# Kernel tuning notes

Hardware: AMD Instinct MI355X
Metric: run time of the kernel (lower is better)

## Reference

```python
import jax, jax.numpy as jnp
import numpy as np

E, H, O = 300, 256, 2            # embedding_size, hidden_size, output_size
N_SENT, SENT_LEN, CLAIM_LEN = 2048, 64, 64


def setup_inputs() -> dict:
    key = jax.random.key(0)
    ks = jax.random.split(key, 24)
    rn = lambda k, shape, s=0.05: (jax.random.normal(k, shape, jnp.float32) * s)
    return {
        "claim": jax.random.normal(ks[0], (CLAIM_LEN, E), jnp.float32),
        "sentences": jax.random.normal(ks[1], (N_SENT, SENT_LEN, E), jnp.float32),
        # claim GRU (PyTorch layout: W_ih (3H,E), W_hh (3H,H), gates ordered r,z,n)
        "Wih_c": rn(ks[2], (3 * H, E)), "Whh_c": rn(ks[3], (3 * H, H)),
        "bih_c": rn(ks[4], (3 * H,)), "bhh_c": rn(ks[5], (3 * H,)),
        # sentence GRU
        "Wih_s": rn(ks[6], (3 * H, E)), "Whh_s": rn(ks[7], (3 * H, H)),
        "bih_s": rn(ks[8], (3 * H,)), "bhh_s": rn(ks[9], (3 * H,)),
        # gates (no bias)
        "Wg_s": rn(ks[10], (1, H)), "Wg_c": rn(ks[11], (1, H)),
        # coherence attention
        "Wac": rn(ks[12], (H, H)), "bac": rn(ks[13], (H,)),
        "Was": rn(ks[14], (1, H)), "bas": rn(ks[15], (1,)),
        # extension linear (H, 2H)
        "Wext": rn(ks[16], (H, 2 * H)), "bext": rn(ks[17], (H,)),
        # joint linear (H, 4H), no bias
        "Wj": rn(ks[18], (H, 4 * H)),
        # entailment attention
        "Wae": rn(ks[19], (1, H)), "bae": rn(ks[20], (1,)),
        # final classifier
        "Wf": rn(ks[21], (O, H)), "bf": rn(ks[22], (O,)),
    }


def _gru_last(x, Wih, Whh, bih, bhh):
    """x: (T, B, E) -> final hidden state (B, H). PyTorch GRU math, zero init."""
    B = x.shape[1]
    Hd = Whh.shape[1]
    gi = jnp.einsum('tbe,ge->tbg', x, Wih) + bih  # (T, B, 3H), input projections

    def step(h, gi_t):
        gh = h @ Whh.T + bhh
        ir, iz, inn = jnp.split(gi_t, 3, axis=-1)
        hr, hz, hn = jnp.split(gh, 3, axis=-1)
        r = jax.nn.sigmoid(ir + hr)
        z = jax.nn.sigmoid(iz + hz)
        n = jnp.tanh(inn + r * hn)
        return (1.0 - z) * n + z * h, None

    h0 = jnp.zeros((B, Hd), x.dtype)
    hT, _ = jax.lax.scan(step, h0, gi)
    return hT


def reference(claim, sentences, Wih_c, Whh_c, bih_c, bhh_c,
              Wih_s, Whh_s, bih_s, bhh_s, Wg_s, Wg_c,
              Wac, bac, Was, bas, Wext, bext, Wj, Wae, bae, Wf, bf):
    # claim encoder: (T,1,E) -> hc (1,H)
    hc = _gru_last(claim[:, None, :], Wih_c, Whh_c, bih_c, bhh_c)
    # batched sentence encoder (replaces the per-sentence Python loop)
    HS = _gru_last(jnp.transpose(sentences, (1, 0, 2)), Wih_s, Whh_s, bih_s, bhh_s)  # (N,H)
    # gated fusion of sentence reps with claim rep
    g = jax.nn.sigmoid(HS @ Wg_s.T + hc @ Wg_c.T)          # (N,1)
    HSg = g * HS + (1.0 - g) * hc                           # (N,H)
    # coherence attention over sentences (row-wise softmax)
    scores = (HSg @ Wac.T + bac) @ HSg.T + (HSg @ Was.T + bas)  # (N,N)
    coh = jax.nn.softmax(scores, axis=1)
    H_apo = coh @ HSg                                       # (N,H)
    H_tilde = jnp.tanh(jnp.concatenate([HS, H_apo], axis=1) @ Wext.T + bext)  # (N,H)
    # joint claim-sentence entailment features (replaces per-row loop)
    hc_b = jnp.broadcast_to(hc, H_tilde.shape)
    joint_in = jnp.concatenate(
        [hc_b, H_tilde, hc * H_tilde, jnp.abs(hc - H_tilde)], axis=1)  # (N,4H)
    H_c_s = jnp.tanh(joint_in @ Wj.T)                       # (N,H)
    # entailment attention (softmax over sentence axis)
    ae = jnp.tanh(H_c_s @ Wae.T + bae)                      # (N,1)
    w = jax.nn.softmax(ae, axis=0)                          # (N,1)
    h_c_S = w.T @ H_c_s                                     # (1,H)
    return jax.nn.sigmoid(h_c_S @ Wf.T + bf)                # (1,O)
```

## Files before the change

kernel.cpp:

```cpp
#include <hip/hip_runtime.h>

typedef unsigned short u16;
typedef unsigned int u32;
typedef short bf16x8 __attribute__((ext_vector_type(8)));
typedef float f32x4 __attribute__((ext_vector_type(4)));
typedef u16 u16x4v __attribute__((ext_vector_type(4)));

__device__ __forceinline__ float b2f(u16 h){ return __uint_as_float(((unsigned)h)<<16); }
__device__ __forceinline__ u16 f2b(float f){
  unsigned u = __float_as_uint(f);
  u += 0x7fffu + ((u>>16)&1u);
  return (u16)(u>>16);
}
__device__ __forceinline__ float sigm(float x){ return 1.f/(1.f+__expf(-x)); }
__device__ __forceinline__ float tanh_(float x){
  float ax=fabsf(x), e=__expf(-2.f*ax), t=(1.f-e)/(1.f+e);
  return x<0.f? -t : t;
}
__device__ __forceinline__ bf16x8 ld8a(const u16* p){
  union{ u16x4v h[2]; bf16x8 v; } u;
  u.h[0]=*(const u16x4v*)p; u.h[1]=*(const u16x4v*)(p+4); return u.v;
}
__device__ __forceinline__ f32x4 mfma16(bf16x8 a, bf16x8 b, f32x4 c){
  return __builtin_amdgcn_mfma_f32_16x16x32_bf16(a,b,c,0,0,0);
}

#define VMW(N)  do{ asm volatile("s_waitcnt vmcnt(" #N ")" ::: "memory"); \
                    __builtin_amdgcn_sched_barrier(0); }while(0)
#define LGK0    do{ asm volatile("s_waitcnt lgkmcnt(0)" ::: "memory"); \
                    __builtin_amdgcn_sched_barrier(0); }while(0)
#define BAR()   do{ asm volatile("" ::: "memory"); __builtin_amdgcn_s_barrier(); \
                    asm volatile("" ::: "memory"); __builtin_amdgcn_sched_barrier(0); }while(0)

__device__ __forceinline__ void gl_lds16(const void* g, void* s){
  __builtin_amdgcn_global_load_lds(
      (const __attribute__((address_space(1))) void*)g,
      (__attribute__((address_space(3))) void*)s, 16, 0, 0);
}
__device__ __forceinline__ void stage_rows(const u16* base, int ld, int kc,
                                           u16* buf, int w, int l){
  #pragma unroll
  for (int ii=0; ii<6; ii++){
    const int i   = w + ii*8;
    const int row = i*16 + (l>>2);
    const int c8  = (l&3) ^ ((row>>2)&3);
    gl_lds16(base + (long)row*ld + kc*32 + c8*8, buf + i*512);
  }
}
__device__ __forceinline__ bf16x8 ldB(const u16* buf, int row, int l){
  const int slot = (l>>4) ^ ((row>>2)&3);
  return *(const bf16x8*)((const char*)buf + row*64 + slot*16);
}

__global__ __launch_bounds__(256) void cvt_kernel(
    const float* __restrict__ WihS, const float* __restrict__ WhhS,
    const float* __restrict__ WihC, const float* __restrict__ WhhC,
    const float* __restrict__ Wac,  const float* __restrict__ Wext,
    const float* __restrict__ Wj,
    const float* __restrict__ bihS, const float* __restrict__ bhhS,
    const float* __restrict__ bihC, const float* __restrict__ bhhC,
    u16* __restrict__ WihP, u16* __restrict__ WhhSb,
    u16* __restrict__ WihCP, u16* __restrict__ WhhCb,
    u16* __restrict__ WacB, u16* __restrict__ WextB, u16* __restrict__ WjB,
    float* __restrict__ biasGI, float* __restrict__ biasGIC)
{
  const int seg = blockIdx.y;
  int n;
  switch(seg){
    case 0: n = 768*320; break;  case 1: n = 196608; break;
    case 2: n = 768*320; break;  case 3: n = 196608; break;
    case 4: n = 65536; break;    case 5: n = 131072; break;
    case 6: n = 262144; break;   default: n = 1536; break;
  }
  for (int i = blockIdx.x*256 + threadIdx.x; i < n; i += gridDim.x*256){
    switch(seg){
      case 0: { int r=i/320, c=i-r*320; WihP[i]  = (c<300)? f2b(WihS[r*300+c]) : (u16)0; } break;
      case 1: WhhSb[i] = f2b(WhhS[i]); break;
      case 2: { int r=i/320, c=i-r*320; WihCP[i] = (c<300)? f2b(WihC[r*300+c]) : (u16)0; } break;
      case 3: WhhCb[i] = f2b(WhhC[i]); break;
      case 4: WacB[i]  = f2b(Wac[i]);  break;
      case 5: WextB[i] = f2b(Wext[i]); break;
      case 6: WjB[i]   = f2b(Wj[i]);   break;
      default:
        if (i < 768) biasGI[i] = bihS[i] + (i < 512 ? bhhS[i] : 0.f);
        else { int j = i - 768; biasGIC[j] = bihC[j] + (j < 512 ? bhhC[j] : 0.f); }
        break;
    }
  }
}

__global__ __launch_bounds__(512) void gi_kernel(
    const int pass,
    const float* __restrict__ sents, const float* __restrict__ claim,
    const u16* __restrict__ WihP, const float* __restrict__ biasGI,
    const u16* __restrict__ WihCP, const float* __restrict__ biasGIC,
    u16* __restrict__ gi_b, float* __restrict__ giC)
{
  __shared__ __align__(16) u16 SA[64*320];
  __shared__ __align__(16) u16 BB[2][768*32];
  const int tid=threadIdx.x, w=tid>>6, l=tid&63, ar=l&15, kg8=(l>>4)*8;
  const f32x4 z4 = {0.f,0.f,0.f,0.f};
  const bool isClaim = (blockIdx.x == 1024);
  const int b = blockIdx.x;

  for (int i=tid; i<64*80; i+=512){
    int r = i/80, q = i - r*80;
    u16x4v o;
    if (q < 75){
      float4 v;
      if (!isClaim) v = ((const float4*)sents)[(long)(2*b + (r>>5))*4800 + (pass*32 + (r&31))*75 + q];
      else          v = ((const float4*)claim)[r*75 + q];
      o[0]=f2b(v.x); o[1]=f2b(v.y); o[2]=f2b(v.z); o[3]=f2b(v.w);
    } else { o[0]=0; o[1]=0; o[2]=0; o[3]=0; }
    int byte = r*640 + q*8; byte ^= (r&7)<<4;
    *(u16x4v*)((char*)SA + byte) = o;
  }
  const u16* Bw = isClaim ? WihCP : WihP;
  stage_rows(Bw, 320, 0, BB[0], w, l);
  stage_rows(Bw, 320, 1, BB[1], w, l);
  LGK0;
  BAR();

  f32x4 acc[24];
  #pragma unroll
  for (int q=0;q<24;q++) acc[q]=z4;

  #pragma unroll
  for (int kc=0;kc<10;kc++){
    if (kc==9) VMW(0); else VMW(6);
    BAR();
    bf16x8 bq[6];
    #pragma unroll
    for (int q=0;q<6;q++) bq[q] = ldB(BB[kc&1], w*96 + q*16 + ar, l);
    #pragma unroll
    for (int m=0;m<4;m++){
      const int abyte = ((m*16+ar)*640 + (kc*32+kg8)*2) ^ ((ar&7)<<4);
      const bf16x8 a = *(const bf16x8*)((const char*)SA + abyte);
      #pragma unroll
      for (int q=0;q<6;q++) acc[m*6+q] = mfma16(a, bq[q], acc[m*6+q]);
    }
    BAR();
    if (kc<8) stage_rows(Bw, 320, kc+2, BB[kc&1], w, l);
  }
  VMW(0);
  const int rb = (l>>4)*4;
  if (!isClaim){
    #pragma unroll
    for (int q=0;q<6;q++){
      const int c = w*96 + q*16 + ar;
      const float bs = biasGI[c];
      #pragma unroll
      for (int m=0;m<4;m++)
        #pragma unroll
        for (int p=0;p<4;p++)
          gi_b[(long)(b*64 + m*16 + rb + p)*768 + c] = f2b(acc[m*6+q][p] + bs);
    }
  } else {
    #pragma unroll
    for (int q=0;q<6;q++){
      const int c = w*96 + q*16 + ar;
      const float bs = biasGIC[c];
      #pragma unroll
      for (int m=0;m<4;m++)
        #pragma unroll
        for (int p=0;p<4;p++)
          giC[(m*16 + rb + p)*768 + c] = acc[m*6+q][p] + bs;
    }
  }
}

__global__ __launch_bounds__(512) void rec_kernel(
    const int pass,
    const u16* __restrict__ gi_b, const u16* __restrict__ WhhSb,
    const float* __restrict__ bhhS,
    float* __restrict__ Hmid, u16* __restrict__ HSout,
    const float* __restrict__ giC, const u16* __restrict__ WhhCb,
    const float* __restrict__ bhhC, const float* __restrict__ Wj,
    const float* __restrict__ WgC,
    float* __restrict__ hcMid, float* __restrict__ hcf,
    float* __restrict__ cvec, float* __restrict__ c0p)
{
  __shared__ __align__(16) u16 Hb[2][16][256];
  __shared__ __align__(16) u16 giL[2][8][776];
  __shared__ float ghL[768];
  __shared__ float hfL[256];
  __shared__ __align__(16) u16 hbL[256];
  const int tid=threadIdx.x, w=tid>>6, l=tid&63, ar=l&15, kg8=(l>>4)*8;
  const f32x4 z4 = {0.f,0.f,0.f,0.f};

  asm volatile("" ::: "v250");

  if (blockIdx.x != 0){
    const long i0 = (long)(blockIdx.x - 1)*8;
    const int rb = (l>>4)*4;
    bf16x8 wf[6][8];
    #pragma unroll
    for (int s=0;s<3;s++)
      #pragma unroll
      for (int ti=0;ti<2;ti++)
        #pragma unroll
        for (int kc=0;kc<8;kc++)
          wf[s*2+ti][kc] = ld8a(WhhSb + (s*256 + w*32 + ti*16 + ar)*256 + kc*32 + kg8);
    const float bhn0 = bhhS[512 + w*32 +  0 + ar];
    const float bhn1 = bhhS[512 + w*32 + 16 + ar];

    for (int i=tid; i<2*16*256; i+=512) ((u16*)Hb)[i] = 0;
    __syncthreads();
    float hold[2][4];
    #pragma unroll
    for (int ti=0;ti<2;ti++)
      #pragma unroll
      for (int p=0;p<4;p++) hold[ti][p] = 0.f;
    if (pass==1 && l<32){
      #pragma unroll
      for (int ti=0;ti<2;ti++){
        #pragma unroll
        for (int p=0;p<4;p++){
          const int c = w*32 + ti*16 + ar, rr = rb + p;
          const float h = Hmid[(i0+rr)*256 + c];
          hold[ti][p] = h;
          const int byte = (rr*512 + c*2) ^ ((rr&7)<<4);
          *(u16*)((char*)&Hb[0][0][0] + byte) = f2b(h);
        }
      }
    }
    const u32* g32 = (const u32*)gi_b;
    u32 pf[6];
    #pragma unroll
    for (int rep=0;rep<6;rep++){
      const int i = rep*512 + tid, j = i/384, cu = i - j*384;
      pf[rep] = g32[((i0+j)*32 + 0)*384 + cu];
    }
    #pragma unroll
    for (int rep=0;rep<6;rep++){
      const int i = rep*512 + tid, j = i/384, cu = i - j*384;
      *(u32*)((char*)&giL[0][0][0] + j*1552 + cu*4) = pf[rep];
    }
    __syncthreads();

    int cur = 0;
    for (int tl=0; tl<32; tl++){
      const int tn = (tl<31) ? tl+1 : 31;
      #pragma unroll
      for (int rep=0;rep<6;rep++){
        const int i = rep*512 + tid, j = i/384, cu = i - j*384;
        pf[rep] = g32[((i0+j)*32 + tn)*384 + cu];
      }
      f32x4 acc[6];
      #pragma unroll
      for (int q=0;q<6;q++) acc[q]=z4;
      if (l < 32){
        #pragma unroll
        for (int s=0;s<2;s++)
          #pragma unroll
          for (int ti=0;ti<2;ti++)
            #pragma unroll
            for (int p=0;p<4;p++){
              const int c = w*32 + ti*16 + ar;
              const u16 v = *(const u16*)((const char*)&giL[cur][0][0] + (rb+p)*1552 + (s*256+c)*2);
              acc[s*2+ti][p] = b2f(v);
            }
      }
      #pragma unroll
      for (int kc=0;kc<8;kc++){
        const int abyte = (ar*512 + (kc*32+kg8)*2) ^ ((ar&7)<<4);
        const bf16x8 a = *(const bf16x8*)((const char*)&Hb[cur][0][0] + abyte);
        #pragma unroll
        for (int q=0;q<6;q++) acc[q] = mfma16(a, wf[q][kc], acc[q]);
      }
      #pragma unroll
      for (int rep=0;rep<6;rep++){
        const int i = rep*512 + tid, j = i/384, cu = i - j*384;
        *(u32*)((char*)&giL[cur^1][0][0] + j*1552 + cu*4) = pf[rep];
      }
      if (l < 32){
        #pragma unroll
        for (int ti=0;ti<2;ti++){
          const int c = w*32 + ti*16 + ar;
          const float bhn = ti ? bhn1 : bhn0;
          #pragma unroll
          for (int p=0;p<4;p++){
            const int rr = rb + p;
            const u16 gv = *(const u16*)((const char*)&giL[cur][0][0] + rr*1552 + (512+c)*2);
            const float r_ = sigm(acc[0+ti][p]);
            const float z_ = sigm(acc[2+ti][p]);
            const float n_ = tanh_(b2f(gv) + r_*(acc[4+ti][p] + bhn));
            const float h = (1.f - z_)*n_ + z_*hold[ti][p];
            hold[ti][p] = h;
            const int byte = (rr*512 + c*2) ^ ((rr&7)<<4);
            *(u16*)((char*)&Hb[cur^1][0][0] + byte) = f2b(h);
          }
        }
      }
      __syncthreads();
      cur ^= 1;
    }
    if (l < 32){
      #pragma unroll
      for (int ti=0;ti<2;ti++){
        #pragma unroll
        for (int p=0;p<4;p++){
          const int c = w*32 + ti*16 + ar, rr = rb + p;
          if (pass==0) Hmid[(i0+rr)*256 + c] = hold[ti][p];
          else         HSout[(i0+rr)*512 + c] = f2b(hold[ti][p]);
        }
      }
    }
  } else {
    const u16* wrow[6];
    #pragma unroll
    for (int q=0;q<6;q++) wrow[q] = WhhCb + (w*96 + q*16 + ar)*256 + kg8;
    if (tid < 256){
      const float h0 = (pass==0) ? 0.f : hcMid[tid];
      hfL[tid] = h0; hbL[tid] = f2b(h0);
    }
    __syncthreads();
    for (int tl=0; tl<32; tl++){
      const int t = pass*32 + tl;
      f32x4 a6[6];
      #pragma unroll
      for (int q=0;q<6;q++) a6[q]=z4;
      #pragma unroll
      for (int kc=0;kc<8;kc++){
        bf16x8 wq[6];
        #pragma unroll
        for (int q=0;q<6;q++) wq[q] = ld8a(wrow[q] + kc*32);
        const bf16x8 a = ld8a((const u16*)hbL + kc*32 + kg8);
        #pragma unroll
        for (int q=0;q<6;q++) a6[q] = mfma16(a, wq[q], a6[q]);
      }
      if (l < 16){
        #pragma unroll
        for (int q=0;q<6;q++) ghL[w*96 + q*16 + l] = a6[q][0];
      }
      __syncthreads();
      if (tid < 256){
        const int c = tid;
        const float r_ = sigm(giC[t*768 +       c] + ghL[c]);
        const float z_ = sigm(giC[t*768 + 256 + c] + ghL[256 + c]);
        const float n_ = tanh_(giC[t*768 + 512 + c] + r_*(ghL[512 + c] + bhhC[512 + c]));
        const float h = (1.f - z_)*n_ + z_*hfL[c];
        hfL[c] = h; hbL[c] = f2b(h);
      }
      __syncthreads();
    }
    if (tid < 256){
      const int c = tid;
      const float hv = hfL[c];
      if (pass == 0) hcMid[c] = hv;
      else {
        hcf[c] = hv;
        float acc2 = 0.f;
        for (int k=0;k<256;k++) acc2 += hfL[k]*Wj[(long)c*1024 + k];
        cvec[c] = acc2;
        if (c==0){ float s=0.f; for (int k=0;k<256;k++) s += hfL[k]*WgC[k]; *c0p = s; }
      }
    }
  }
}

__global__ __launch_bounds__(256) void fusion_kernel(
    const u16* __restrict__ HSH, const float* __restrict__ Wgs,
    const float* __restrict__ hcf, const float* __restrict__ c0p,
    u16* __restrict__ HSg, u16* __restrict__ HSgT)
{
  __shared__ float gbuf[64];
  __shared__ __align__(16) u16 tile[64][258];
  const int tid=threadIdx.x, w=tid>>6, l=tid&63;
  const long i0 = (long)blockIdx.x * 64;
  const float c0 = *c0p;
  for (int rr=0; rr<16; rr++){
    long i = i0 + w*16 + rr;
    float p = 0.f;
    for (int c=l; c<256; c+=64) p += b2f(HSH[i*512+c]) * Wgs[c];
    for (int o=32;o;o>>=1) p += __shfl_down(p,o,64);
    if (l==0) gbuf[w*16+rr] = sigm(p + c0);
  }
  __syncthreads();
  for (int idx=tid; idx<64*256; idx+=256){
    int r = idx>>8, c = idx&255;
    float g = gbuf[r];
    float hs = b2f(HSH[(i0+r)*512 + c]);
    u16 bv = f2b(g*hs + (1.f-g)*hcf[c]);
    HSg[(i0+r)*256 + c] = bv;
    tile[r][c] = bv;
  }
  __syncthreads();
  const int ioff = tid&63, cg = tid>>6;
  for (int cc=cg; cc<256; cc+=4)
    HSgT[(long)cc*2048 + i0 + ioff] = tile[ioff][cc];
}

template<int MODE>
__global__ __launch_bounds__(256) void gemmk(
    const u16* __restrict__ A, long lda,
    const u16* __restrict__ Bw, long ldb,
    void* __restrict__ Cp, long ldc, int K,
    const float* __restrict__ biasf,
    const float* __restrict__ hc)
{
  const int tid=threadIdx.x, w=tid>>6, l=tid&63, ar=l&15, kg8=(l>>4)*8;
  const long row0 = (long)blockIdx.x*64 + w*16;
  const long col0 = (long)blockIdx.y*64;
  const f32x4 z4 = {0.f,0.f,0.f,0.f};
  f32x4 acc[4] = {z4,z4,z4,z4};
  const u16* ap = A + (row0+ar)*lda + kg8;
  const u16* bp0 = Bw + (col0+ 0+ar)*ldb + kg8;
  const u16* bp1 = Bw + (col0+16+ar)*ldb + kg8;
  const u16* bp2 = Bw + (col0+32+ar)*ldb + kg8;
  const u16* bp3 = Bw + (col0+48+ar)*ldb + kg8;
  for (int k0=0; k0<K; k0+=32){
    bf16x8 a = ld8a(ap + k0);
    acc[0] = mfma16(a, ld8a(bp0+k0), acc[0]);
    acc[1] = mfma16(a, ld8a(bp1+k0), acc[1]);
    acc[2] = mfma16(a, ld8a(bp2+k0), acc[2]);
    acc[3] = mfma16(a, ld8a(bp3+k0), acc[3]);
  }
  const int rbase = (l>>4)*4;
  #pragma unroll
  for (int t=0;t<4;t++){
    long c = col0 + t*16 + ar;
    #pragma unroll
    for (int p=0;p<4;p++){
      long r = row0 + rbase + p;
      float v = acc[t][p];
      if constexpr (MODE==0){
        if (biasf) v += biasf[c];
        ((u16*)Cp)[r*ldc + c] = f2b(v);
      } else if constexpr (MODE==1){
        ((float*)Cp)[r*ldc + c] = v;
      } else if constexpr (MODE==2){
        float tv = tanh_(v + biasf[c]);
        u16* Uo = (u16*)Cp;
        float hv = hc[c];
        Uo[r*768 + c]       = f2b(tv);
        Uo[r*768 + 256 + c] = f2b(hv*tv);
        Uo[r*768 + 512 + c] = f2b(fabsf(hv - tv));
      } else {
        float tv = tanh_(v + biasf[c]);
        ((u16*)Cp)[r*ldc + c] = f2b(tv);
      }
    }
  }
}

__global__ __launch_bounds__(256) void softmax_rows(float* __restrict__ S)
{
  __shared__ float buf[2048];
  __shared__ float red[4];
  const long i = blockIdx.x;
  float* row = S + i*2048;
  const int tid = threadIdx.x;
  float m = -1e30f;
  for (int c=tid; c<2048; c+=256){ float v=row[c]; buf[c]=v; m=fmaxf(m,v); }
  for (int o=32;o;o>>=1) m = fmaxf(m, __shfl_down(m,o,64));
  if ((tid&63)==0) red[tid>>6] = m;
  __syncthreads();
  m = fmaxf(fmaxf(red[0],red[1]), fmaxf(red[2],red[3]));
  __syncthreads();
  float s = 0.f;
  for (int c=tid; c<2048; c+=256){ float e=__expf(buf[c]-m); buf[c]=e; s+=e; }
  for (int o=32;o;o>>=1) s += __shfl_down(s,o,64);
  if ((tid&63)==0) red[tid>>6] = s;
  __syncthreads();
  s = red[0]+red[1]+red[2]+red[3];
  const float rinv = 1.f/s;
  u16* P = (u16*)S + i*4096;
  for (int c=tid; c<2048; c+=256) P[c] = f2b(buf[c]*rinv);
}

__global__ __launch_bounds__(256) void ae_kernel(
    const u16* __restrict__ Hcs, const float* __restrict__ Wae, const float* __restrict__ bae,
    float* __restrict__ part, float* __restrict__ psum)
{
  __shared__ float aebuf[64];
  const int b=blockIdx.x, tid=threadIdx.x, w=tid>>6, l=tid&63;
  const long i0 = (long)b*64;
  const float baev = bae[0];
  for (int rr=0; rr<16; rr++){
    long i = i0 + w*16 + rr;
    float p = 0.f;
    for (int c=l; c<256; c+=64) p += b2f(Hcs[i*256+c]) * Wae[c];
    for (int o=32;o;o>>=1) p += __shfl_down(p,o,64);
    if (l==0) aebuf[w*16+rr] = __expf(tanh_(p + baev));
  }
  __syncthreads();
  float acc = 0.f;
  const int c = tid;
  for (int r=0;r<64;r++) acc += aebuf[r] * b2f(Hcs[(i0+r)*256 + c]);
  part[b*256 + c] = acc;
  if (tid==0){ float s=0.f; for (int r=0;r<64;r++) s+=aebuf[r]; psum[b]=s; }
}

__global__ __launch_bounds__(256) void final_kernel(
    const float* __restrict__ part, const float* __restrict__ psum,
    const float* __restrict__ Wf, const float* __restrict__ bf_, float* __restrict__ out)
{
  __shared__ float hbuf[256];
  __shared__ float ssum;
  const int tid = threadIdx.x;
  float v = 0.f;
  for (int b=0;b<32;b++) v += part[b*256 + tid];
  hbuf[tid] = v;
  if (tid==0){ float s=0.f; for (int b=0;b<32;b++) s+=psum[b]; ssum=s; }
  __syncthreads();
  const int w = tid>>6, l = tid&63;
  if (w < 2){
    float rinv = 1.f/ssum;
    float p = 0.f;
    for (int c=l; c<256; c+=64) p += hbuf[c]*rinv*Wf[w*256 + c];
    for (int o=32;o;o>>=1) p += __shfl_down(p,o,64);
    if (l==0) out[w] = sigm(p + bf_[w]);
  }
}

extern "C" void kernel_launch(void* const* d_in, const int* in_sizes, int n_in,
                              void* d_out, int out_size, void* d_ws, size_t ws_size,
                              hipStream_t stream)
{
  const float* claim=(const float*)d_in[0];
  const float* sents=(const float*)d_in[1];
  const float* WihC =(const float*)d_in[2];
  const float* WhhC =(const float*)d_in[3];
  const float* bihC =(const float*)d_in[4];
  const float* bhhC =(const float*)d_in[5];
  const float* WihS =(const float*)d_in[6];
  const float* WhhS =(const float*)d_in[7];
  const float* bihS =(const float*)d_in[8];
  const float* bhhS =(const float*)d_in[9];
  const float* WgS  =(const float*)d_in[10];
  const float* WgC  =(const float*)d_in[11];
  const float* Wac  =(const float*)d_in[12];
  const float* bac  =(const float*)d_in[13];
  const float* Wext =(const float*)d_in[16];
  const float* bext =(const float*)d_in[17];
  const float* Wj   =(const float*)d_in[18];
  const float* Wae  =(const float*)d_in[19];
  const float* bae  =(const float*)d_in[20];
  const float* Wf   =(const float*)d_in[21];
  const float* bf_  =(const float*)d_in[22];

  char* ws = (char*)d_ws;
  size_t off = 0;
  auto alloc = [&](size_t b)->void*{ void* p = ws + off; off = (off + b + 255) & ~(size_t)255; return p; };
  float* hcf  = (float*)alloc(256*4);
  float* cvec = (float*)alloc(256*4);
  float* c0p  = (float*)alloc(16);
  float* hcMid= (float*)alloc(256*4);
  float* giC  = (float*)alloc((size_t)64*768*4);
  u16* WihP   = (u16*)alloc((size_t)768*320*2);
  u16* WhhSb  = (u16*)alloc((size_t)196608*2);
  u16* WihCP  = (u16*)alloc((size_t)768*320*2);
  u16* WhhCb  = (u16*)alloc((size_t)196608*2);
  u16* WacB   = (u16*)alloc((size_t)65536*2);
  u16* WextB  = (u16*)alloc((size_t)131072*2);
  u16* WjB    = (u16*)alloc((size_t)262144*2);
  float* biasGI  = (float*)alloc(768*4);
  float* biasGIC = (float*)alloc(768*4);
  u16* HSH  = (u16*)alloc((size_t)2048*512*2);
  u16* HSg  = (u16*)alloc((size_t)2048*256*2);
  u16* HSgT = (u16*)alloc((size_t)256*2048*2);
  u16* A1   = (u16*)alloc((size_t)2048*256*2);
  u16* Up   = (u16*)alloc((size_t)2048*768*2);
  u16* Hcs  = (u16*)alloc((size_t)2048*256*2);
  float* part = (float*)alloc(32*256*4);
  float* psum = (float*)alloc(32*4);
  float* Hmid = (float*)alloc((size_t)2048*256*4);
  u16* gi_b   = (u16*)alloc((size_t)65536*768*2);
  float* S    = (float*)gi_b;

  cvt_kernel<<<dim3(960,8),256,0,stream>>>(WihS,WhhS,WihC,WhhC,Wac,Wext,Wj,
                                           bihS,bhhS,bihC,bhhC,
                                           WihP,WhhSb,WihCP,WhhCb,WacB,WextB,WjB,
                                           biasGI,biasGIC);
  gi_kernel<<<1025,512,0,stream>>>(0,sents,claim,WihP,biasGI,WihCP,biasGIC,gi_b,giC);
  rec_kernel<<<257,512,0,stream>>>(0,gi_b,WhhSb,bhhS,Hmid,HSH,
                                   giC,WhhCb,bhhC,Wj,WgC,hcMid,hcf,cvec,c0p);
  gi_kernel<<<1024,512,0,stream>>>(1,sents,claim,WihP,biasGI,WihCP,biasGIC,gi_b,giC);
  rec_kernel<<<257,512,0,stream>>>(1,gi_b,WhhSb,bhhS,Hmid,HSH,
                                   giC,WhhCb,bhhC,Wj,WgC,hcMid,hcf,cvec,c0p);

  fusion_kernel<<<32,256,0,stream>>>(HSH,WgS,hcf,c0p,HSg,HSgT);
  gemmk<0><<<dim3(32,4),256,0,stream>>>(HSg,256L,WacB,256L,(void*)A1,256L,256,bac,nullptr);
  gemmk<1><<<dim3(32,32),256,0,stream>>>(A1,256L,HSg,256L,(void*)S,2048L,256,nullptr,nullptr);
  softmax_rows<<<2048,256,0,stream>>>(S);
  gemmk<0><<<dim3(32,4),256,0,stream>>>((const u16*)S,4096L,HSgT,2048L,(void*)(HSH+256),512L,2048,nullptr,nullptr);
  gemmk<2><<<dim3(32,4),256,0,stream>>>(HSH,512L,WextB,512L,(void*)Up,768L,512,bext,hcf);
  gemmk<3><<<dim3(32,4),256,0,stream>>>(Up,768L,WjB+256,1024L,(void*)Hcs,256L,768,cvec,nullptr);
  ae_kernel<<<32,256,0,stream>>>(Hcs,Wae,bae,part,psum);
  final_kernel<<<1,256,0,stream>>>(part,psum,Wf,bf_,(float*)d_out);
}
```

Before: 800.5 us.

## Overlap second-half input projection with first-half GRU recurrence in one launch

Adds a combined kernel in which blocks 1-256 run the first 32 timesteps of the sentence GRU recurrence while extra blocks (257+) compute the input-gate projections for timesteps 32-63 into a second buffer. This lets the latency-bound recurrence share the GPU with the compute-bound GEMM instead of running them back to back. It needs a second large gi buffer and falls back to the old sequence when workspace is too small. Co-scheduled projection blocks may contend for CUs and memory bandwidth with the recurrence blocks.

Result: slower. 861.0 us (+7.6%).

```diff
diff --git a/kernel.cpp b/kernel.cpp
--- a/kernel.cpp
+++ b/kernel.cpp
@@ -187,7 +187,6 @@
   __shared__ __align__(16) u16 hbL[256];
   const int tid=threadIdx.x, w=tid>>6, l=tid&63, ar=l&15, kg8=(l>>4)*8;
   const f32x4 z4 = {0.f,0.f,0.f,0.f};
-
   asm volatile("" ::: "v250");
 
   if (blockIdx.x != 0){
@@ -356,6 +355,209 @@
         if (c==0){ float s=0.f; for (int k=0;k<256;k++) s += hfL[k]*WgC[k]; *c0p = s; }
       }
     }
+  }
+}
+
+__global__ __launch_bounds__(512) void recgi_kernel(
+    const u16* __restrict__ gi_bA, const u16* __restrict__ WhhSb,
+    const float* __restrict__ bhhS, float* __restrict__ Hmid,
+    const float* __restrict__ giC, const u16* __restrict__ WhhCb,
+    const float* __restrict__ bhhC, float* __restrict__ hcMid,
+    const float* __restrict__ sents, const u16* __restrict__ WihP,
+    const float* __restrict__ biasGI, u16* __restrict__ gi_bB)
+{
+  __shared__ __align__(16) char SM[45824];
+  const int tid=threadIdx.x, w=tid>>6, l=tid&63, ar=l&15, kg8=(l>>4)*8;
+  const f32x4 z4 = {0.f,0.f,0.f,0.f};
+  asm volatile("" ::: "v250");
+
+  if (blockIdx.x >= 257){
+    u16* SA = (u16*)SM;
+    const int b = blockIdx.x - 257;
+    for (int i=tid; i<64*80; i+=512){
+      int r = i/80, q = i - r*80;
+      u16x4v o;
+      if (q < 75){
+        const float4 v = ((const float4*)sents)[(long)(2*b + (r>>5))*4800 + (32 + (r&31))*75 + q];
+        o[0]=f2b(v.x); o[1]=f2b(v.y); o[2]=f2b(v.z); o[3]=f2b(v.w);
+      } else { o[0]=0; o[1]=0; o[2]=0; o[3]=0; }
+      int byte = r*640 + q*8; byte ^= (r&7)<<4;
+      *(u16x4v*)((char*)SA + byte) = o;
+    }
+    __syncthreads();
+    const u16* brow[6];
+    #pragma unroll
+    for (int q=0;q<6;q++) brow[q] = WihP + (w*96 + q*16 + ar)*320 + kg8;
+    f32x4 acc[24];
+    #pragma unroll
+    for (int q=0;q<24;q++) acc[q]=z4;
+    #pragma unroll
+    for (int kc=0;kc<10;kc++){
+      bf16x8 bq[6];
+      #pragma unroll
+      for (int q=0;q<6;q++) bq[q] = ld8a(brow[q] + kc*32);
+      #pragma unroll
+      for (int m=0;m<4;m++){
+        const int abyte = ((m*16+ar)*640 + (kc*32+kg8)*2) ^ ((ar&7)<<4);
+        const bf16x8 a = *(const bf16x8*)((const char*)SA + abyte);
+        #pragma unroll
+        for (int q=0;q<6;q++) acc[m*6+q] = mfma16(a, bq[q], acc[m*6+q]);
+      }
+    }
+    const int rb = (l>>4)*4;
+    #pragma unroll
+    for (int q=0;q<6;q++){
+      const int c = w*96 + q*16 + ar;
+      const float bs = biasGI[c];
+      #pragma unroll
+      for (int m=0;m<4;m++)
+        #pragma unroll
+        for (int p=0;p<4;p++)
+          gi_bB[(long)(b*64 + m*16 + rb + p)*768 + c] = f2b(acc[m*6+q][p] + bs);
+    }
+  } else if (blockIdx.x != 0){
+    u16*  HbP  = (u16*)SM;
+    u16*  giLp = (u16*)(SM + 16384);
+    const long i0 = (long)(blockIdx.x - 1)*8;
+    const int rb = (l>>4)*4;
+    bf16x8 wf[6][8];
+    #pragma unroll
+    for (int s=0;s<3;s++)
+      #pragma unroll
+      for (int ti=0;ti<2;ti++)
+        #pragma unroll
+        for (int kc=0;kc<8;kc++)
+          wf[s*2+ti][kc] = ld8a(WhhSb + (s*256 + w*32 + ti*16 + ar)*256 + kc*32 + kg8);
+    const float bhn0 = bhhS[512 + w*32 +  0 + ar];
+    const float bhn1 = bhhS[512 + w*32 + 16 + ar];
+
+    for (int i=tid; i<2*16*256; i+=512) HbP[i] = 0;
+    __syncthreads();
+    float hold[2][4];
+    #pragma unroll
+    for (int ti=0;ti<2;ti++)
+      #pragma unroll
+      for (int p=0;p<4;p++) hold[ti][p] = 0.f;
+    const u32* g32 = (const u32*)gi_bA;
+    u32 pf[6];
+    #pragma unroll
+    for (int rep=0;rep<6;rep++){
+      const int i = rep*512 + tid, j = i/384, cu = i - j*384;
+      pf[rep] = g32[((i0+j)*32 + 0)*384 + cu];
+    }
+    #pragma unroll
+    for (int rep=0;rep<6;rep++){
+      const int i = rep*512 + tid, j = i/384, cu = i - j*384;
+      *(u32*)((char*)giLp + j*1552 + cu*4) = pf[rep];
+    }
+    __syncthreads();
+
+    int cur = 0;
+    for (int tl=0; tl<32; tl++){
+      const int tn = (tl<31) ? tl+1 : 31;
+      #pragma unroll
+      for (int rep=0;rep<6;rep++){
+        const int i = rep*512 + tid, j = i/384, cu = i - j*384;
+        pf[rep] = g32[((i0+j)*32 + tn)*384 + cu];
+      }
+      f32x4 acc[6];
+      #pragma unroll
+      for (int q=0;q<6;q++) acc[q]=z4;
+      if (l < 32){
+        #pragma unroll
+        for (int s=0;s<2;s++)
+          #pragma unroll
+          for (int ti=0;ti<2;ti++)
+            #pragma unroll
+            for (int p=0;p<4;p++){
+              const int c = w*32 + ti*16 + ar;
+              const u16 v = *(const u16*)((const char*)giLp + cur*12416 + (rb+p)*1552 + (s*256+c)*2);
+              acc[s*2+ti][p] = b2f(v);
+            }
+      }
+      #pragma unroll
+      for (int kc=0;kc<8;kc++){
+        const int abyte = (ar*512 + (kc*32+kg8)*2) ^ ((ar&7)<<4);
+        const bf16x8 a = *(const bf16x8*)((const char*)HbP + cur*8192 + abyte);
+        #pragma unroll
+        for (int q=0;q<6;q++) acc[q] = mfma16(a, wf[q][kc], acc[q]);
+      }
+      #pragma unroll
+      for (int rep=0;rep<6;rep++){
+        const int i = rep*512 + tid, j = i/384, cu = i - j*384;
+        *(u32*)((char*)giLp + (cur^1)*12416 + j*1552 + cu*4) = pf[rep];
+      }
+      if (l < 32){
+        #pragma unroll
+        for (int ti=0;ti<2;ti++){
+          const int c = w*32 + ti*16 + ar;
+          const float bhn = ti ? bhn1 : bhn0;
+          #pragma unroll
+          for (int p=0;p<4;p++){
+            const int rr = rb + p;
+            const u16 gv = *(const u16*)((const char*)giLp + cur*12416 + rr*1552 + (512+c)*2);
+            const float r_ = sigm(acc[0+ti][p]);
+            const float z_ = sigm(acc[2+ti][p]);
+            const float n_ = tanh_(b2f(gv) + r_*(acc[4+ti][p] + bhn));
+            const float h = (1.f - z_)*n_ + z_*hold[ti][p];
+            hold[ti][p] = h;
+            const int byte = (rr*512 + c*2) ^ ((rr&7)<<4);
+            *(u16*)((char*)HbP + (cur^1)*8192 + byte) = f2b(h);
+          }
+        }
+      }
+      __syncthreads();
+      cur ^= 1;
+    }
+    if (l < 32){
+      #pragma unroll
+      for (int ti=0;ti<2;ti++){
+        #pragma unroll
+        for (int p=0;p<4;p++){
+          const int c = w*32 + ti*16 + ar, rr = rb + p;
+          Hmid[(i0+rr)*256 + c] = hold[ti][p];
+        }
+      }
+    }
+  } else {
+    float* ghL = (float*)(SM + 41216);
+    float* hfL = (float*)(SM + 44288);
+    u16*   hbL = (u16*)(SM + 45312);
+    const u16* wrow[6];
+    #pragma unroll
+    for (int q=0;q<6;q++) wrow[q] = WhhCb + (w*96 + q*16 + ar)*256 + kg8;
+    if (tid < 256){ hfL[tid] = 0.f; hbL[tid] = 0; }
+    __syncthreads();
+    for (int tl=0; tl<32; tl++){
+      const int t = tl;
+      f32x4 a6[6];
+      #pragma unroll
+      for (int q=0;q<6;q++) a6[q]=z4;
+      #pragma unroll
+      for (int kc=0;kc<8;kc++){
+        bf16x8 wq[6];
+        #pragma unroll
+        for (int q=0;q<6;q++) wq[q] = ld8a(wrow[q] + kc*32);
+        const bf16x8 a = ld8a((const u16*)hbL + kc*32 + kg8);
+        #pragma unroll
+        for (int q=0;q<6;q++) a6[q] = mfma16(a, wq[q], a6[q]);
+      }
+      if (l < 16){
+        #pragma unroll
+        for (int q=0;q<6;q++) ghL[w*96 + q*16 + l] = a6[q][0];
+      }
+      __syncthreads();
+      if (tid < 256){
+        const int c = tid;
+        const float r_ = sigm(giC[t*768 +       c] + ghL[c]);
+        const float z_ = sigm(giC[t*768 + 256 + c] + ghL[256 + c]);
+        const float n_ = tanh_(giC[t*768 + 512 + c] + r_*(ghL[512 + c] + bhhC[512 + c]));
+        const float h = (1.f - z_)*n_ + z_*hfL[c];
+        hfL[c] = h; hbL[c] = f2b(h);
+      }
+      __syncthreads();
+    }
+    if (tid < 256) hcMid[tid] = hfL[tid];
   }
 }
 
@@ -566,19 +768,29 @@
   float* part = (float*)alloc(32*256*4);
   float* psum = (float*)alloc(32*4);
   float* Hmid = (float*)alloc((size_t)2048*256*4);
-  u16* gi_b   = (u16*)alloc((size_t)65536*768*2);
-  float* S    = (float*)gi_b;
+  const size_t GIB = (size_t)65536*768*2;
+  u16* gi_bA  = (u16*)alloc(GIB);
+  float* S    = (float*)gi_bA;
+  const bool overlap = (off + GIB) <= ws_size;
+  u16* gi_bB  = overlap ? (u16*)alloc(GIB) : gi_bA;
 
   cvt_kernel<<<dim3(960,8),256,0,stream>>>(WihS,WhhS,WihC,WhhC,Wac,Wext,Wj,
                                            bihS,bhhS,bihC,bhhC,
                                            WihP,WhhSb,WihCP,WhhCb,WacB,WextB,WjB,
                                            biasGI,biasGIC);
-  gi_kernel<<<1025,512,0,stream>>>(0,sents,claim,WihP,biasGI,WihCP,biasGIC,gi_b,giC);
-  rec_kernel<<<257,512,0,stream>>>(0,gi_b,WhhSb,bhhS,Hmid,HSH,
-                                   giC,WhhCb,bhhC,Wj,WgC,hcMid,hcf,cvec,c0p);
-  gi_kernel<<<1024,512,0,stream>>>(1,sents,claim,WihP,biasGI,WihCP,biasGIC,gi_b,giC);
-  rec_kernel<<<257,512,0,stream>>>(1,gi_b,WhhSb,bhhS,Hmid,HSH,
-                                   giC,WhhCb,bhhC,Wj,WgC,hcMid,hcf,cvec,c0p);
+  gi_kernel<<<1025,512,0,stream>>>(0,sents,claim,WihP,biasGI,WihCP,biasGIC,gi_bA,giC);
+  if (overlap){
+    recgi_kernel<<<1281,512,0,stream>>>(gi_bA,WhhSb,bhhS,Hmid,giC,WhhCb,bhhC,hcMid,
+                                        sents,WihP,biasGI,gi_bB);
+    rec_kernel<<<257,512,0,stream>>>(1,gi_bB,WhhSb,bhhS,Hmid,HSH,
+                                     giC,WhhCb,bhhC,Wj,WgC,hcMid,hcf,cvec,c0p);
+  } else {
+    rec_kernel<<<257,512,0,stream>>>(0,gi_bA,WhhSb,bhhS,Hmid,HSH,
+                                     giC,WhhCb,bhhC,Wj,WgC,hcMid,hcf,cvec,c0p);
+    gi_kernel<<<1024,512,0,stream>>>(1,sents,claim,WihP,biasGI,WihCP,biasGIC,gi_bA,giC);
+    rec_kernel<<<257,512,0,stream>>>(1,gi_bA,WhhSb,bhhS,Hmid,HSH,
+                                     giC,WhhCb,bhhC,Wj,WgC,hcMid,hcf,cvec,c0p);
+  }
 
   fusion_kernel<<<32,256,0,stream>>>(HSH,WgS,hcf,c0p,HSg,HSgT);
   gemmk<0><<<dim3(32,4),256,0,stream>>>(HSg,256L,WacB,256L,(void*)A1,256L,256,bac,nullptr);
```

## Merge two-pass GRU input projection and recurrence into single launches

Applied to the files above, without the earlier changes.

Both time halves of the sentence input projection are computed in one gi_kernel launch with 2049 blocks, writing to two separate buffers. The recurrence now walks all 64 steps in one rec_kernel launch with an internal phase loop. This removes two kernel launches, the fp32 round trip of the mid-sequence hidden state through global memory, and the second load of the recurrent weights into registers. In exchange it needs a second ~100MB workspace buffer. The fallback path used when the workspace is too small looks wrong: the second gi pass overwrites the single buffer before the recurrence reads the first half.

Result: slower. 895.7 us (+11.9%).

```diff
diff --git a/kernel.cpp b/kernel.cpp
--- a/kernel.cpp
+++ b/kernel.cpp
@@ -90,18 +90,21 @@
 }
 
 __global__ __launch_bounds__(512) void gi_kernel(
-    const int pass,
+    const int claimb,
     const float* __restrict__ sents, const float* __restrict__ claim,
     const u16* __restrict__ WihP, const float* __restrict__ biasGI,
     const u16* __restrict__ WihCP, const float* __restrict__ biasGIC,
-    u16* __restrict__ gi_b, float* __restrict__ giC)
+    u16* __restrict__ giA, u16* __restrict__ giB, float* __restrict__ giC,
+    const int basePass)
 {
   __shared__ __align__(16) u16 SA[64*320];
   __shared__ __align__(16) u16 BB[2][768*32];
   const int tid=threadIdx.x, w=tid>>6, l=tid&63, ar=l&15, kg8=(l>>4)*8;
   const f32x4 z4 = {0.f,0.f,0.f,0.f};
-  const bool isClaim = (blockIdx.x == 1024);
-  const int b = blockIdx.x;
+  const bool isClaim = ((int)blockIdx.x == claimb);
+  const int pass = isClaim ? 0 : (blockIdx.x >= 1024 ? 1 : basePass);
+  const int b = isClaim ? 0 : (blockIdx.x >= 1024 ? blockIdx.x - 1024 : blockIdx.x);
+  u16* gout = (pass ? giB : giA);
 
   for (int i=tid; i<64*80; i+=512){
     int r = i/80, q = i - r*80;
@@ -153,7 +156,7 @@
       for (int m=0;m<4;m++)
         #pragma unroll
         for (int p=0;p<4;p++)
-          gi_b[(long)(b*64 + m*16 + rb + p)*768 + c] = f2b(acc[m*6+q][p] + bs);
+          gout[(long)(b*64 + m*16 + rb + p)*768 + c] = f2b(acc[m*6+q][p] + bs);
     }
   } else {
     #pragma unroll
@@ -170,15 +173,13 @@
 }
 
 __global__ __launch_bounds__(512) void rec_kernel(
-    const int pass,
-    const u16* __restrict__ gi_b, const u16* __restrict__ WhhSb,
-    const float* __restrict__ bhhS,
-    float* __restrict__ Hmid, u16* __restrict__ HSout,
+    const u16* __restrict__ giA, const u16* __restrict__ giB,
+    const u16* __restrict__ WhhSb, const float* __restrict__ bhhS,
+    u16* __restrict__ HSout,
     const float* __restrict__ giC, const u16* __restrict__ WhhCb,
     const float* __restrict__ bhhC, const float* __restrict__ Wj,
     const float* __restrict__ WgC,
-    float* __restrict__ hcMid, float* __restrict__ hcf,
-    float* __restrict__ cvec, float* __restrict__ c0p)
+    float* __restrict__ hcf, float* __restrict__ cvec, float* __restrict__ c0p)
 {
   __shared__ __align__(16) u16 Hb[2][16][256];
   __shared__ __align__(16) u16 giL[2][8][776];
@@ -187,7 +188,6 @@
   __shared__ __align__(16) u16 hbL[256];
   const int tid=threadIdx.x, w=tid>>6, l=tid&63, ar=l&15, kg8=(l>>4)*8;
   const f32x4 z4 = {0.f,0.f,0.f,0.f};
-
   asm volatile("" ::: "v250");
 
   if (blockIdx.x != 0){
@@ -205,104 +205,94 @@
     const float bhn1 = bhhS[512 + w*32 + 16 + ar];
 
     for (int i=tid; i<2*16*256; i+=512) ((u16*)Hb)[i] = 0;
+    float hold[2][4];
+    #pragma unroll
+    for (int ti=0;ti<2;ti++)
+      #pragma unroll
+      for (int p=0;p<4;p++) hold[ti][p] = 0.f;
     __syncthreads();
-    float hold[2][4];
-    #pragma unroll
-    for (int ti=0;ti<2;ti++)
-      #pragma unroll
-      for (int p=0;p<4;p++) hold[ti][p] = 0.f;
-    if (pass==1 && l<32){
+
+    #pragma unroll 1
+    for (int ph=0; ph<2; ph++){
+      const u32* g32 = (const u32*)(ph ? giB : giA);
+      u32 pf[6];
+      #pragma unroll
+      for (int rep=0;rep<6;rep++){
+        const int i = rep*512 + tid, j = i/384, cu = i - j*384;
+        pf[rep] = g32[((i0+j)*32 + 0)*384 + cu];
+      }
+      #pragma unroll
+      for (int rep=0;rep<6;rep++){
+        const int i = rep*512 + tid, j = i/384, cu = i - j*384;
+        *(u32*)((char*)&giL[0][0][0] + j*1552 + cu*4) = pf[rep];
+      }
+      __syncthreads();
+
+      int cur = 0;
+      for (int tl=0; tl<32; tl++){
+        const int tn = (tl<31) ? tl+1 : 31;
+        #pragma unroll
+        for (int rep=0;rep<6;rep++){
+          const int i = rep*512 + tid, j = i/384, cu = i - j*384;
+          pf[rep] = g32[((i0+j)*32 + tn)*384 + cu];
+        }
+        f32x4 acc[6];
+        #pragma unroll
+        for (int q=0;q<6;q++) acc[q]=z4;
+        if (l < 32){
+          #pragma unroll
+          for (int s=0;s<2;s++)
+            #pragma unroll
+            for (int ti=0;ti<2;ti++)
+              #pragma unroll
+              for (int p=0;p<4;p++){
+                const int c = w*32 + ti*16 + ar;
+                const u16 v = *(const u16*)((const char*)&giL[cur][0][0] + (rb+p)*1552 + (s*256+c)*2);
+                acc[s*2+ti][p] = b2f(v);
+              }
+        }
+        #pragma unroll
+        for (int kc=0;kc<8;kc++){
+          const int abyte = (ar*512 + (kc*32+kg8)*2) ^ ((ar&7)<<4);
+          const bf16x8 a = *(const bf16x8*)((const char*)&Hb[cur][0][0] + abyte);
+          #pragma unroll
+          for (int q=0;q<6;q++) acc[q] = mfma16(a, wf[q][kc], acc[q]);
+        }
+        #pragma unroll
+        for (int rep=0;rep<6;rep++){
+          const int i = rep*512 + tid, j = i/384, cu = i - j*384;
+          *(u32*)((char*)&giL[cur^1][0][0] + j*1552 + cu*4) = pf[rep];
+        }
+        if (l < 32){
+          #pragma unroll
+          for (int ti=0;ti<2;ti++){
+            const int c = w*32 + ti*16 + ar;
+            const float bhn = ti ? bhn1 : bhn0;
+            #pragma unroll
+            for (int p=0;p<4;p++){
+              const int rr = rb + p;
+              const u16 gv = *(const u16*)((const char*)&giL[cur][0][0] + rr*1552 + (512+c)*2);
+              const float r_ = sigm(acc[0+ti][p]);
+              const float z_ = sigm(acc[2+ti][p]);
+              const float n_ = tanh_(b2f(gv) + r_*(acc[4+ti][p] + bhn));
+              const float h = (1.f - z_)*n_ + z_*hold[ti][p];
+              hold[ti][p] = h;
+              const int byte = (rr*512 + c*2) ^ ((rr&7)<<4);
+              *(u16*)((char*)&Hb[cur^1][0][0] + byte) = f2b(h);
+            }
+          }
+        }
+        __syncthreads();
+        cur ^= 1;
+      }
+    }
+    if (l < 32){
       #pragma unroll
       for (int ti=0;ti<2;ti++){
         #pragma unroll
         for (int p=0;p<4;p++){
           const int c = w*32 + ti*16 + ar, rr = rb + p;
-          const float h = Hmid[(i0+rr)*256 + c];
-          hold[ti][p] = h;
-          const int byte = (rr*512 + c*2) ^ ((rr&7)<<4);
-          *(u16*)((char*)&Hb[0][0][0] + byte) = f2b(h);
-        }
-      }
-    }
-    const u32* g32 = (const u32*)gi_b;
-    u32 pf[6];
-    #pragma unroll
-    for (int rep=0;rep<6;rep++){
-      const int i = rep*512 + tid, j = i/384, cu = i - j*384;
-      pf[rep] = g32[((i0+j)*32 + 0)*384 + cu];
-    }
-    #pragma unroll
-    for (int rep=0;rep<6;rep++){
-      const int i = rep*512 + tid, j = i/384, cu = i - j*384;
-      *(u32*)((char*)&giL[0][0][0] + j*1552 + cu*4) = pf[rep];
-    }
-    __syncthreads();
-
-    int cur = 0;
-    for (int tl=0; tl<32; tl++){
-      const int tn = (tl<31) ? tl+1 : 31;
-      #pragma unroll
-      for (int rep=0;rep<6;rep++){
-        const int i = rep*512 + tid, j = i/384, cu = i - j*384;
-        pf[rep] = g32[((i0+j)*32 + tn)*384 + cu];
-      }
-      f32x4 acc[6];
-      #pragma unroll
-      for (int q=0;q<6;q++) acc[q]=z4;
-      if (l < 32){
-        #pragma unroll
-        for (int s=0;s<2;s++)
-          #pragma unroll
-          for (int ti=0;ti<2;ti++)
-            #pragma unroll
-            for (int p=0;p<4;p++){
-              const int c = w*32 + ti*16 + ar;
-              const u16 v = *(const u16*)((const char*)&giL[cur][0][0] + (rb+p)*1552 + (s*256+c)*2);
-              acc[s*2+ti][p] = b2f(v);
-            }
-      }
-      #pragma unroll
-      for (int kc=0;kc<8;kc++){
-        const int abyte = (ar*512 + (kc*32+kg8)*2) ^ ((ar&7)<<4);
-        const bf16x8 a = *(const bf16x8*)((const char*)&Hb[cur][0][0] + abyte);
-        #pragma unroll
-        for (int q=0;q<6;q++) acc[q] = mfma16(a, wf[q][kc], acc[q]);
-      }
-      #pragma unroll
-      for (int rep=0;rep<6;rep++){
-        const int i = rep*512 + tid, j = i/384, cu = i - j*384;
-        *(u32*)((char*)&giL[cur^1][0][0] + j*1552 + cu*4) = pf[rep];
-      }
-      if (l < 32){
-        #pragma unroll
-        for (int ti=0;ti<2;ti++){
-          const int c = w*32 + ti*16 + ar;
-          const float bhn = ti ? bhn1 : bhn0;
-          #pragma unroll
-          for (int p=0;p<4;p++){
-            const int rr = rb + p;
-            const u16 gv = *(const u16*)((const char*)&giL[cur][0][0] + rr*1552 + (512+c)*2);
-            const float r_ = sigm(acc[0+ti][p]);
-            const float z_ = sigm(acc[2+ti][p]);
-            const float n_ = tanh_(b2f(gv) + r_*(acc[4+ti][p] + bhn));
-            const float h = (1.f - z_)*n_ + z_*hold[ti][p];
-            hold[ti][p] = h;
-            const int byte = (rr*512 + c*2) ^ ((rr&7)<<4);
-            *(u16*)((char*)&Hb[cur^1][0][0] + byte) = f2b(h);
-          }
-        }
-      }
-      __syncthreads();
-      cur ^= 1;
-    }
-    if (l < 32){
-      #pragma unroll
-      for (int ti=0;ti<2;ti++){
-        #pragma unroll
-        for (int p=0;p<4;p++){
-          const int c = w*32 + ti*16 + ar, rr = rb + p;
-          if (pass==0) Hmid[(i0+rr)*256 + c] = hold[ti][p];
-          else         HSout[(i0+rr)*512 + c] = f2b(hold[ti][p]);
+          HSout[(i0+rr)*512 + c] = f2b(hold[ti][p]);
         }
       }
     }
@@ -310,13 +300,9 @@
     const u16* wrow[6];
     #pragma unroll
     for (int q=0;q<6;q++) wrow[q] = WhhCb + (w*96 + q*16 + ar)*256 + kg8;
-    if (tid < 256){
-      const float h0 = (pass==0) ? 0.f : hcMid[tid];
-      hfL[tid] = h0; hbL[tid] = f2b(h0);
-    }
+    if (tid < 256){ hfL[tid] = 0.f; hbL[tid] = 0; }
     __syncthreads();
-    for (int tl=0; tl<32; tl++){
-      const int t = pass*32 + tl;
+    for (int t=0; t<64; t++){
       f32x4 a6[6];
       #pragma unroll
       for (int q=0;q<6;q++) a6[q]=z4;
@@ -346,15 +332,11 @@
     }
     if (tid < 256){
       const int c = tid;
-      const float hv = hfL[c];
-      if (pass == 0) hcMid[c] = hv;
-      else {
-        hcf[c] = hv;
-        float acc2 = 0.f;
-        for (int k=0;k<256;k++) acc2 += hfL[k]*Wj[(long)c*1024 + k];
-        cvec[c] = acc2;
-        if (c==0){ float s=0.f; for (int k=0;k<256;k++) s += hfL[k]*WgC[k]; *c0p = s; }
-      }
+      hcf[c] = hfL[c];
+      float acc2 = 0.f;
+      for (int k=0;k<256;k++) acc2 += hfL[k]*Wj[(long)c*1024 + k];
+      cvec[c] = acc2;
+      if (c==0){ float s=0.f; for (int k=0;k<256;k++) s += hfL[k]*WgC[k]; *c0p = s; }
     }
   }
 }
@@ -546,7 +528,6 @@
   float* hcf  = (float*)alloc(256*4);
   float* cvec = (float*)alloc(256*4);
   float* c0p  = (float*)alloc(16);
-  float* hcMid= (float*)alloc(256*4);
   float* giC  = (float*)alloc((size_t)64*768*4);
   u16* WihP   = (u16*)alloc((size_t)768*320*2);
   u16* WhhSb  = (u16*)alloc((size_t)196608*2);
@@ -565,20 +546,29 @@
   u16* Hcs  = (u16*)alloc((size_t)2048*256*2);
   float* part = (float*)alloc(32*256*4);
   float* psum = (float*)alloc(32*4);
-  float* Hmid = (float*)alloc((size_t)2048*256*4);
-  u16* gi_b   = (u16*)alloc((size_t)65536*768*2);
-  float* S    = (float*)gi_b;
+  const size_t GIB = (size_t)65536*768*2;
+  u16* gi_bA  = (u16*)alloc(GIB);
+  float* S    = (float*)gi_bA;
+  const bool merged = (off + GIB) <= ws_size;
+  u16* gi_bB  = merged ? (u16*)alloc(GIB) : gi_bA;
 
   cvt_kernel<<<dim3(960,8),256,0,stream>>>(WihS,WhhS,WihC,WhhC,Wac,Wext,Wj,
                                            bihS,bhhS,bihC,bhhC,
                                            WihP,WhhSb,WihCP,WhhCb,WacB,WextB,WjB,
                                            biasGI,biasGIC);
-  gi_kernel<<<1025,512,0,stream>>>(0,sents,claim,WihP,biasGI,WihCP,biasGIC,gi_b,giC);
-  rec_kernel<<<257,512,0,stream>>>(0,gi_b,WhhSb,bhhS,Hmid,HSH,
-                                   giC,WhhCb,bhhC,Wj,WgC,hcMid,hcf,cvec,c0p);
-  gi_kernel<<<1024,512,0,stream>>>(1,sents,claim,WihP,biasGI,WihCP,biasGIC,gi_b,giC);
-  rec_kernel<<<257,512,0,stream>>>(1,gi_b,WhhSb,bhhS,Hmid,HSH,
-                                   giC,WhhCb,bhhC,Wj,WgC,hcMid,hcf,cvec,c0p);
+  if (merged){
+    gi_kernel<<<2049,512,0,stream>>>(2048,sents,claim,WihP,biasGI,WihCP,biasGIC,
+                                     gi_bA,gi_bB,giC,0);
+    rec_kernel<<<257,512,0,stream>>>(gi_bA,gi_bB,WhhSb,bhhS,HSH,
+                                     giC,WhhCb,bhhC,Wj,WgC,hcf,cvec,c0p);
+  } else {
+    gi_kernel<<<1025,512,0,stream>>>(1024,sents,claim,WihP,biasGI,WihCP,biasGIC,
+                                     gi_bA,gi_bA,giC,0);
+    gi_kernel<<<1024,512,0,stream>>>(-1,sents,claim,WihP,biasGI,WihCP,biasGIC,
+                                     gi_bA,gi_bA,giC,1);
+    rec_kernel<<<257,512,0,stream>>>(gi_bA,gi_bA,WhhSb,bhhS,HSH,
+                                     giC,WhhCb,bhhC,Wj,WgC,hcf,cvec,c0p);
+  }
 
   fusion_kernel<<<32,256,0,stream>>>(HSH,WgS,hcf,c0p,HSg,HSgT);
   gemmk<0><<<dim3(32,4),256,0,stream>>>(HSg,256L,WacB,256L,(void*)A1,256L,256,bac,nullptr);
```
